# Performance work log

Measured on AMD Instinct MI355X. Metric: run time of the kernel, lower is better.

The kernel has to match this reference:

```python
import jax, jax.numpy as jnp
import numpy as np

N = 50000; E = 800000; B = 5000
ND = 32; ED = 16; HD = 64; H = 128; L = 3
IN_DIM = ND + 2 * H  # 288, GNN in_channels
NEG = 0.2  # GATv2 leaky_relu slope
EPS = 1e-5  # LayerNorm eps


def silu(x):
    return x * jax.nn.sigmoid(x)


def layer_norm(x, g, b):
    mu = jnp.mean(x, -1, keepdims=True)
    v = jnp.var(x, -1, keepdims=True)
    return (x - mu) * jax.lax.rsqrt(v + EPS) * g + b


def setup_inputs() -> dict:
    key = jax.random.key(0)
    ks = iter(jax.random.split(key, 48))

    def w(shape):
        return jax.random.normal(next(ks), shape, jnp.float32) * 0.02

    inp = {}
    inp['x_t'] = jax.random.normal(next(ks), (N, ND), jnp.float32)
    inp['t'] = jax.random.randint(next(ks), (N,), 0, 1000)
    inp['household_features'] = jax.random.normal(next(ks), (B, HD), jnp.float32)
    inp['edge_index'] = jax.random.randint(next(ks), (2, E), 0, N)
    inp['edge_attr'] = jax.random.normal(next(ks), (E, ED), jnp.float32)
    inp['batch'] = jnp.sort(jax.random.randint(next(ks), (N,), 0, B))
    z = jnp.zeros; o = jnp.ones
    inp.update(dict(
        tW1=w((1, H)), tb1=z(H), tW2=w((H, H)), tb2=z(H),
        hW1=w((HD, H)), hb1=z(H), hg1=o(H), hB1=z(H),
        hW2=w((H, H)), hb2=z(H), hg2=o(H), hB2=z(H),
        Wl=w((L, IN_DIM, H)), bl=z((L, H)), Wr=w((L, IN_DIM, H)), br=z((L, H)),
        We=w((L, ED, H)), att=w((L, H)), gb=z((L, H)),
        fcpW=w((H, IN_DIM)), fcpb=z(IN_DIM),
        npW1=w((H, H)), npb1=z(H), npg=o(H), npB=z(H),
        npW2=w((H, ND)), npb2=z(ND)))
    return inp


def reference(x_t, t, household_features, edge_index, edge_attr, batch,
              tW1, tb1, tW2, tb2,
              hW1, hb1, hg1, hB1, hW2, hb2, hg2, hB2,
              Wl, bl, Wr, br, We, att, gb,
              fcpW, fcpb, npW1, npb1, npg, npB, npW2, npb2):
    # time embedding: Linear(1,H) -> SiLU -> Linear(H,H)
    t_emb = silu(t[:, None].astype(jnp.float32) @ tW1 + tb1) @ tW2 + tb2
    # household encoder: (Linear, LN, SiLU) x2, then gather per node
    h = silu(layer_norm(household_features @ hW1 + hb1, hg1, hB1))
    h = silu(layer_norm(h @ hW2 + hb2, hg2, hB2))
    x = jnp.concatenate([x_t, t_emb, h[batch]], axis=1)  # [N, IN_DIM]

    # add self loops (PyG default), edge_attr filled with per-feature mean
    loop = jnp.arange(N)
    src = jnp.concatenate([edge_index[0], loop])
    dst = jnp.concatenate([edge_index[1], loop])
    ea = jnp.concatenate([edge_attr, jnp.broadcast_to(edge_attr.mean(0), (N, ED))], axis=0)

    for l in range(L):  # GATv2Conv layers (heads=1)
        xl = x @ Wl[l] + bl[l]  # [N, H] source transform
        xr = x @ Wr[l] + br[l]  # [N, H] target transform
        m = jax.nn.leaky_relu(xl[src] + xr[dst] + ea @ We[l], NEG)  # [Etot, H]
        score = m @ att[l]  # [Etot]
        smax = jax.ops.segment_max(score, dst, num_segments=N)
        ex = jnp.exp(score - smax[dst])
        denom = jax.ops.segment_sum(ex, dst, num_segments=N) + 1e-16
        alpha = ex / denom[dst]
        out = jax.ops.segment_sum(alpha[:, None] * xl[src], dst, num_segments=N) + gb[l]
        x = silu(out)
        if l < L - 1:
            x = x @ fcpW + fcpb  # fc_projection back to IN_DIM
    # node_projection: Linear, LN, SiLU, Linear
    return silu(layer_norm(x @ npW1 + npb1, npg, npB)) @ npW2 + npb2
```

## Files before the change

kernel.cpp:

```cpp
#include <hip/hip_runtime.h>
#include <hip/hip_bf16.h>

#define NN 50000
#define NE 800000
#define NB 5000
#define ND 32
#define EDD 16
#define HDD 64
#define H 128
#define ETOT (NE + NN)
#define NEG 0.2f
#define EPS_LN 1e-5f

__device__ __forceinline__ float siluf(float x){ return x / (1.f + __expf(-x)); }

__device__ __forceinline__ float wsum(float v){
  v += __shfl_xor(v, 32, 64);
  v += __shfl_xor(v, 16, 64);
  v += __shfl_xor(v, 8, 64);
  v += __shfl_xor(v, 4, 64);
  v += __shfl_xor(v, 2, 64);
  v += __shfl_xor(v, 1, 64);
  return v;
}

__device__ __forceinline__ float blockLN128(float x, const float* g, const float* b, int j, float* red){
  int lane = j & 63, wid = j >> 6;
  float s = wsum(x);
  if (lane == 0) red[wid] = s;
  __syncthreads();
  float mu = (red[0] + red[1]) * 0.0078125f;
  float d = x - mu;
  float s2 = wsum(d * d);
  if (lane == 0) red[2 + wid] = s2;
  __syncthreads();
  float var = (red[2] + red[3]) * 0.0078125f;
  return d * (1.f / sqrtf(var + EPS_LN)) * g[j] + b[j];
}

__global__ __launch_bounds__(128) void k_house(const float* __restrict__ hf,
    const float* __restrict__ hW1, const float* __restrict__ hb1,
    const float* __restrict__ hg1, const float* __restrict__ hB1,
    const float* __restrict__ hW2, const float* __restrict__ hb2,
    const float* __restrict__ hg2, const float* __restrict__ hB2,
    float* __restrict__ hout){
  __shared__ float sin_[HDD];
  __shared__ float smid[H];
  __shared__ float red[4];
  int bidx = blockIdx.x, j = threadIdx.x;
  if (j < HDD) sin_[j] = hf[bidx * HDD + j];
  __syncthreads();
  float acc = hb1[j];
  #pragma unroll
  for (int k = 0; k < HDD; k++) acc += sin_[k] * hW1[k * H + j];
  float v = siluf(blockLN128(acc, hg1, hB1, j, red));
  __syncthreads();
  smid[j] = v;
  __syncthreads();
  float acc2 = hb2[j];
  #pragma unroll
  for (int k = 0; k < H; k++) acc2 += smid[k] * hW2[k * H + j];
  float v2 = siluf(blockLN128(acc2, hg2, hB2, j, red));
  hout[bidx * H + j] = v2;
}

__global__ __launch_bounds__(128) void k_temb(const float* __restrict__ tW1, const float* __restrict__ tb1,
    const float* __restrict__ tW2, const float* __restrict__ tb2, float* __restrict__ table){
  __shared__ float smid[H];
  int bidx = blockIdx.x, j = threadIdx.x;
  float tv = (float)bidx;
  smid[j] = siluf(tv * tW1[j] + tb1[j]);
  __syncthreads();
  float acc = tb2[j];
  #pragma unroll
  for (int k = 0; k < H; k++) acc += smid[k] * tW2[k * H + j];
  table[bidx * H + j] = acc;
}

__global__ __launch_bounds__(256) void k_gemm(const float* __restrict__ A, const float* __restrict__ W,
    const float* __restrict__ bias, float* __restrict__ C, int M, int K, int Nc){
  __shared__ float As[16][68];
  __shared__ float Ws[16][64];
  int t = threadIdx.x;
  int m0 = blockIdx.x * 64, n0 = blockIdx.y * 64;
  int tx = t & 15, ty = t >> 4;
  int la_m = t >> 2, la_k = (t & 3) << 2;
  int lw_k = t >> 4, lw_j = (t & 15) << 2;
  float acc[4][4] = {{0.f}};
  int arow = m0 + la_m;
  for (int k0 = 0; k0 < K; k0 += 16){
    float4 a = make_float4(0.f, 0.f, 0.f, 0.f);
    if (arow < M) a = *(const float4*)(A + (size_t)arow * K + k0 + la_k);
    As[la_k + 0][la_m] = a.x; As[la_k + 1][la_m] = a.y;
    As[la_k + 2][la_m] = a.z; As[la_k + 3][la_m] = a.w;
    float4 wv = make_float4(0.f, 0.f, 0.f, 0.f);
    if (n0 + lw_j < Nc) wv = *(const float4*)(W + (size_t)(k0 + lw_k) * Nc + n0 + lw_j);
    *(float4*)&Ws[lw_k][lw_j] = wv;
    __syncthreads();
    #pragma unroll
    for (int k = 0; k < 16; k++){
      float4 a4 = *(const float4*)&As[k][ty << 2];
      float4 b4 = *(const float4*)&Ws[k][tx << 2];
      acc[0][0] += a4.x * b4.x; acc[0][1] += a4.x * b4.y; acc[0][2] += a4.x * b4.z; acc[0][3] += a4.x * b4.w;
      acc[1][0] += a4.y * b4.x; acc[1][1] += a4.y * b4.y; acc[1][2] += a4.y * b4.z; acc[1][3] += a4.y * b4.w;
      acc[2][0] += a4.z * b4.x; acc[2][1] += a4.z * b4.y; acc[2][2] += a4.z * b4.z; acc[2][3] += a4.z * b4.w;
      acc[3][0] += a4.w * b4.x; acc[3][1] += a4.w * b4.y; acc[3][2] += a4.w * b4.z; acc[3][3] += a4.w * b4.w;
    }
    __syncthreads();
  }
  int col = n0 + (tx << 2);
  if (col < Nc){
    float4 b4 = make_float4(0.f, 0.f, 0.f, 0.f);
    if (bias) b4 = *(const float4*)(bias + col);
    #pragma unroll
    for (int r = 0; r < 4; r++){
      int row = m0 + (ty << 2) + r;
      if (row < M){
        float4 o = make_float4(acc[r][0] + b4.x, acc[r][1] + b4.y, acc[r][2] + b4.z, acc[r][3] + b4.w);
        *(float4*)(C + (size_t)row * Nc + col) = o;
      }
    }
  }
}

__global__ void k_pack0(const float* __restrict__ Wl, const float* __restrict__ Wr,
    float* __restrict__ Whead, float* __restrict__ Wmid, float* __restrict__ Wtail){
  int r = blockIdx.x, c = threadIdx.x;
  float v = (c < H) ? Wl[r * H + c] : Wr[r * H + (c - H)];
  if (r < 32) Whead[r * 256 + c] = v;
  else if (r < 160) Wmid[(r - 32) * 256 + c] = v;
  else Wtail[(r - 160) * 256 + c] = v;
}
__global__ void k_packW(const float* __restrict__ Wl, const float* __restrict__ Wr, float* __restrict__ Wp){
  int r = blockIdx.x, c = threadIdx.x;
  Wp[r * 256 + c] = (c < H) ? Wl[r * H + c] : Wr[r * H + (c - H)];
}
__global__ void k_bias0(const float* __restrict__ bl, const float* __restrict__ br, float* __restrict__ b0){
  int c = threadIdx.x;
  b0[c] = (c < H) ? bl[c] : br[c - H];
}
__global__ void k_cvec(const float* __restrict__ fcpb, const float* __restrict__ Wp,
    const float* __restrict__ bl, const float* __restrict__ br, float* __restrict__ cc){
  int c = threadIdx.x;
  float acc = (c < H) ? bl[c] : br[c - H];
  for (int k = 0; k < 288; k++) acc += fcpb[k] * Wp[k * 256 + c];
  cc[c] = acc;
}

__global__ __launch_bounds__(256) void k_xlr0(const float* __restrict__ x_t, const int* __restrict__ t,
    const int* __restrict__ batch, const float* __restrict__ T0, const float* __restrict__ H0,
    const float* __restrict__ Whead, const float* __restrict__ b0, float* __restrict__ xlr){
  __shared__ float sx[ND];
  __shared__ int sti, sbi;
  int i = blockIdx.x, c = threadIdx.x;
  if (c < ND) sx[c] = x_t[i * ND + c];
  if (c == 0){ sti = t[i]; sbi = batch[i]; }
  __syncthreads();
  float acc = b0[c] + T0[(size_t)sti * 256 + c] + H0[(size_t)sbi * 256 + c];
  #pragma unroll
  for (int k = 0; k < ND; k++) acc += sx[k] * Whead[k * 256 + c];
  xlr[(size_t)i * 256 + c] = acc;
}

__global__ void k_edge_mean(const float* __restrict__ ea, float* __restrict__ sum16){
  __shared__ float ss[16];
  int t = threadIdx.x;
  if (t < 16) ss[t] = 0.f;
  __syncthreads();
  float p[16];
  #pragma unroll
  for (int k = 0; k < 16; k++) p[k] = 0.f;
  for (int r = blockIdx.x * blockDim.x + t; r < NE; r += gridDim.x * blockDim.x){
    const float4* rp = (const float4*)(ea + (size_t)r * 16);
    float4 q0 = rp[0], q1 = rp[1], q2 = rp[2], q3 = rp[3];
    p[0] += q0.x; p[1] += q0.y; p[2] += q0.z; p[3] += q0.w;
    p[4] += q1.x; p[5] += q1.y; p[6] += q1.z; p[7] += q1.w;
    p[8] += q2.x; p[9] += q2.y; p[10] += q2.z; p[11] += q2.w;
    p[12] += q3.x; p[13] += q3.y; p[14] += q3.z; p[15] += q3.w;
  }
  #pragma unroll
  for (int k = 0; k < 16; k++) atomicAdd(&ss[k], p[k]);
  __syncthreads();
  if (t < 16) atomicAdd(&sum16[t], ss[t]);
}
__global__ void k_mean_scale(float* sum16){
  sum16[threadIdx.x] *= (1.f / NE);
}

__global__ void k_deg_init(int* __restrict__ deg){
  int i = blockIdx.x * 256 + threadIdx.x;
  if (i < NN) deg[i] = 1;
}
__global__ void k_deg_count(const int* __restrict__ eidx, int* __restrict__ deg){
  int e = blockIdx.x * 256 + threadIdx.x;
  if (e < NE) atomicAdd(&deg[eidx[NE + e]], 1);
}
__global__ __launch_bounds__(256) void k_scan1(const int* __restrict__ deg, int* __restrict__ row_ptr, int* __restrict__ bs){
  __shared__ int sc[256];
  int t = threadIdx.x;
  int base = blockIdx.x * 1024 + t * 4;
  int v0 = (base + 0 < NN) ? deg[base + 0] : 0;
  int v1 = (base + 1 < NN) ? deg[base + 1] : 0;
  int v2 = (base + 2 < NN) ? deg[base + 2] : 0;
  int v3 = (base + 3 < NN) ? deg[base + 3] : 0;
  int s0 = v0, s1 = s0 + v1, s2 = s1 + v2, s3 = s2 + v3;
  sc[t] = s3;
  __syncthreads();
  for (int off = 1; off < 256; off <<= 1){
    int add = (t >= off) ? sc[t - off] : 0;
    __syncthreads();
    sc[t] += add;
    __syncthreads();
  }
  int excl = sc[t] - s3;
  if (base + 0 < NN) row_ptr[base + 1] = excl + s0;
  if (base + 1 < NN) row_ptr[base + 2] = excl + s1;
  if (base + 2 < NN) row_ptr[base + 3] = excl + s2;
  if (base + 3 < NN) row_ptr[base + 4] = excl + s3;
  if (t == 255) bs[blockIdx.x] = sc[255];
}
__global__ void k_scan2(int* __restrict__ bs, int nb){
  int lane = threadIdx.x;
  int v = (lane < nb) ? bs[lane] : 0;
  for (int off = 1; off < 64; off <<= 1){
    int n = __shfl_up(v, off, 64);
    if (lane >= off) v += n;
  }
  if (lane < nb) bs[lane] = v;
}
__global__ void k_scan3(int* __restrict__ row_ptr, const int* __restrict__ bs){
  int i = blockIdx.x * 256 + threadIdx.x;
  if (i == 0) row_ptr[0] = 0;
  if (i < NN){
    int chunk = i >> 10;
    if (chunk > 0) row_ptr[i + 1] += bs[chunk - 1];
  }
}
__global__ void k_fill_init(const int* __restrict__ row_ptr, int* __restrict__ fill){
  int i = blockIdx.x * 256 + threadIdx.x;
  if (i < NN) fill[i] = row_ptr[i];
}
__global__ void k_fill_edges(const int* __restrict__ eidx, int* __restrict__ fill,
    int* __restrict__ csrc, int* __restrict__ ceid){
  int e = blockIdx.x * 256 + threadIdx.x;
  if (e < NE){
    int d = eidx[NE + e];
    int pos = atomicAdd(&fill[d], 1);
    csrc[pos] = eidx[e];
    ceid[pos] = e;
  }
}
__global__ void k_fill_self(int* __restrict__ fill, int* __restrict__ csrc, int* __restrict__ ceid){
  int i = blockIdx.x * 256 + threadIdx.x;
  if (i < NN){
    int pos = atomicAdd(&fill[i], 1);
    csrc[pos] = i;
    ceid[pos] = NE;
  }
}

__global__ __launch_bounds__(256) void k_sagg(const float* __restrict__ xlr,
    const float* __restrict__ ea, const float* __restrict__ eamean,
    const float* __restrict__ Wel, const float* __restrict__ attl, const float* __restrict__ gbl,
    const int* __restrict__ row_ptr, const int* __restrict__ csrc, const int* __restrict__ ceid,
    float* __restrict__ y){
  int t = threadIdx.x;
  int wid = t >> 6, lane = t & 63;
  int i = blockIdx.x * 4 + wid;
  if (i >= NN) return;
  int dim = lane << 1;
  float2 rW[16];
  #pragma unroll
  for (int k = 0; k < 16; k++) rW[k] = *(const float2*)(Wel + k * H + dim);
  float ewm0 = 0.f, ewm1 = 0.f;
  #pragma unroll
  for (int k = 0; k < 16; k++){ float mk = eamean[k]; ewm0 += mk * rW[k].x; ewm1 += mk * rW[k].y; }
  float2 xr = *(const float2*)(xlr + (size_t)i * 256 + H + dim);
  float a0 = attl[dim], a1 = attl[dim + 1];
  int row = __builtin_amdgcn_readfirstlane(row_ptr[i]);
  int end = __builtin_amdgcn_readfirstlane(row_ptr[i + 1]);
  float m = -1e30f, den = 0.f, ax = 0.f, ay = 0.f;
  for (int p = row; p < end; ++p){
    int s   = __builtin_amdgcn_readfirstlane(csrc[p]);
    int eid = __builtin_amdgcn_readfirstlane(ceid[p]);
    float2 vl = *(const float2*)(xlr + (size_t)s * 256 + dim);
    float ew0, ew1;
    if (eid < NE){
      const float* ep = ea + (size_t)eid * 16;
      ew0 = 0.f; ew1 = 0.f;
      #pragma unroll
      for (int k = 0; k < 16; k++){ float evk = ep[k]; ew0 += evk * rW[k].x; ew1 += evk * rW[k].y; }
    } else { ew0 = ewm0; ew1 = ewm1; }
    float vx = vl.x + xr.x + ew0;
    float vy = vl.y + xr.y + ew1;
    vx = fmaxf(vx, NEG * vx);
    vy = fmaxf(vy, NEG * vy);
    float sc = wsum(a0 * vx + a1 * vy);
    float newm = fmaxf(m, sc);
    float scale = __expf(m - newm);
    float wv = __expf(sc - newm);
    den = den * scale + wv;
    ax = ax * scale + wv * vl.x;
    ay = ay * scale + wv * vl.y;
    m = newm;
  }
  float inv = 1.f / (den + 1e-16f);
  float ox = siluf(ax * inv + gbl[dim]);
  float oy = siluf(ay * inv + gbl[dim + 1]);
  *(float2*)(y + (size_t)i * H + dim) = make_float2(ox, oy);
}

__global__ __launch_bounds__(128) void k_ln_silu(const float* __restrict__ z, const float* __restrict__ g,
    const float* __restrict__ b, float* __restrict__ z2){
  __shared__ float red[4];
  int i = blockIdx.x, j = threadIdx.x;
  float x = z[(size_t)i * H + j];
  float v = blockLN128(x, g, b, j, red);
  z2[(size_t)i * H + j] = siluf(v);
}

extern "C" void kernel_launch(void* const* d_in, const int* in_sizes, int n_in,
                              void* d_out, int out_size, void* d_ws, size_t ws_size,
                              hipStream_t stream){
  (void)in_sizes; (void)n_in; (void)out_size; (void)ws_size;
  const float* x_t  = (const float*)d_in[0];
  const int*   t    = (const int*)d_in[1];
  const float* hf   = (const float*)d_in[2];
  const int*   eidx = (const int*)d_in[3];
  const float* ea   = (const float*)d_in[4];
  const int*   batch= (const int*)d_in[5];
  const float* tW1  = (const float*)d_in[6];
  const float* tb1  = (const float*)d_in[7];
  const float* tW2  = (const float*)d_in[8];
  const float* tb2  = (const float*)d_in[9];
  const float* hW1  = (const float*)d_in[10];
  const float* hb1  = (const float*)d_in[11];
  const float* hg1  = (const float*)d_in[12];
  const float* hB1  = (const float*)d_in[13];
  const float* hW2  = (const float*)d_in[14];
  const float* hb2  = (const float*)d_in[15];
  const float* hg2  = (const float*)d_in[16];
  const float* hB2  = (const float*)d_in[17];
  const float* Wl   = (const float*)d_in[18];
  const float* bl   = (const float*)d_in[19];
  const float* Wr   = (const float*)d_in[20];
  const float* br   = (const float*)d_in[21];
  const float* We   = (const float*)d_in[22];
  const float* att  = (const float*)d_in[23];
  const float* gb   = (const float*)d_in[24];
  const float* fcpW = (const float*)d_in[25];
  const float* fcpb = (const float*)d_in[26];
  const float* npW1 = (const float*)d_in[27];
  const float* npb1 = (const float*)d_in[28];
  const float* npg  = (const float*)d_in[29];
  const float* npB  = (const float*)d_in[30];
  const float* npW2 = (const float*)d_in[31];
  const float* npb2 = (const float*)d_in[32];

  char* w = (char*)d_ws;
  size_t off = 0;
  auto alloc = [&](size_t bytes) -> void* {
    void* p = w + off;
    off += (bytes + 255) & ~(size_t)255;
    return p;
  };
  float* table = (float*)alloc((size_t)1000 * H * 4);
  float* hbuf  = (float*)alloc((size_t)NB * H * 4);
  float* T0    = (float*)alloc((size_t)1000 * 256 * 4);
  float* H0b   = (float*)alloc((size_t)NB * 256 * 4);
  float* W0h   = (float*)alloc((size_t)32 * 256 * 4);
  float* W0m   = (float*)alloc((size_t)128 * 256 * 4);
  float* W0t   = (float*)alloc((size_t)128 * 256 * 4);
  float* b0    = (float*)alloc(256 * 4);
  float* Wp1   = (float*)alloc((size_t)288 * 256 * 4);
  float* Wp2   = (float*)alloc((size_t)288 * 256 * 4);
  float* Ac1   = (float*)alloc((size_t)128 * 256 * 4);
  float* Ac2   = (float*)alloc((size_t)128 * 256 * 4);
  float* cc1   = (float*)alloc(256 * 4);
  float* cc2   = (float*)alloc(256 * 4);
  float* eam   = (float*)alloc(16 * 4);
  int* deg     = (int*)alloc((size_t)NN * 4);
  int* row_ptr = (int*)alloc((size_t)(NN + 1) * 4);
  int* fill    = (int*)alloc((size_t)NN * 4);
  int* bs      = (int*)alloc(64 * 4);
  int* csrc    = (int*)alloc((size_t)ETOT * 4);
  int* ceid    = (int*)alloc((size_t)ETOT * 4);
  float* xlr   = (float*)alloc((size_t)NN * 256 * 4);
  float* y     = (float*)alloc((size_t)NN * H * 4);
  float* z  = xlr;
  float* z2 = xlr + (size_t)NN * H;

  hipMemsetAsync(eam, 0, 64, stream);
  k_edge_mean<<<512, 256, 0, stream>>>(ea, eam);
  k_mean_scale<<<1, 16, 0, stream>>>(eam);
  k_house<<<NB, 128, 0, stream>>>(hf, hW1, hb1, hg1, hB1, hW2, hb2, hg2, hB2, hbuf);
  k_temb<<<1000, 128, 0, stream>>>(tW1, tb1, tW2, tb2, table);
  k_deg_init<<<(NN + 255) / 256, 256, 0, stream>>>(deg);
  k_deg_count<<<(NE + 255) / 256, 256, 0, stream>>>(eidx, deg);
  k_scan1<<<49, 256, 0, stream>>>(deg, row_ptr, bs);
  k_scan2<<<1, 64, 0, stream>>>(bs, 49);
  k_scan3<<<(NN + 255) / 256, 256, 0, stream>>>(row_ptr, bs);
  k_fill_init<<<(NN + 255) / 256, 256, 0, stream>>>(row_ptr, fill);
  k_fill_edges<<<(NE + 255) / 256, 256, 0, stream>>>(eidx, fill, csrc, ceid);
  k_fill_self<<<(NN + 255) / 256, 256, 0, stream>>>(fill, csrc, ceid);
  k_pack0<<<288, 256, 0, stream>>>(Wl, Wr, W0h, W0m, W0t);
  k_bias0<<<1, 256, 0, stream>>>(bl, br, b0);
  k_packW<<<288, 256, 0, stream>>>(Wl + 1 * 288 * H, Wr + 1 * 288 * H, Wp1);
  k_packW<<<288, 256, 0, stream>>>(Wl + 2 * 288 * H, Wr + 2 * 288 * H, Wp2);
  k_cvec<<<1, 256, 0, stream>>>(fcpb, Wp1, bl + H, br + H, cc1);
  k_cvec<<<1, 256, 0, stream>>>(fcpb, Wp2, bl + 2 * H, br + 2 * H, cc2);
  auto gemm = [&](const float* A, const float* W_, const float* bias, float* C, int M, int K, int Nc){
    dim3 g((M + 63) / 64, (Nc + 63) / 64);
    k_gemm<<<g, 256, 0, stream>>>(A, W_, bias, C, M, K, Nc);
  };
  gemm(table, W0m, nullptr, T0, 1000, H, 256);
  gemm(hbuf, W0t, nullptr, H0b, NB, H, 256);
  gemm(fcpW, Wp1, nullptr, Ac1, H, 288, 256);
  gemm(fcpW, Wp2, nullptr, Ac2, H, 288, 256);
  k_xlr0<<<NN, 256, 0, stream>>>(x_t, t, batch, T0, H0b, W0h, b0, xlr);
  k_sagg<<<(NN + 3) / 4, 256, 0, stream>>>(xlr, ea, eam, We, att, gb, row_ptr, csrc, ceid, y);
  gemm(y, Ac1, cc1, xlr, NN, H, 256);
  k_sagg<<<(NN + 3) / 4, 256, 0, stream>>>(xlr, ea, eam, We + 16 * H, att + H, gb + H, row_ptr, csrc, ceid, y);
  gemm(y, Ac2, cc2, xlr, NN, H, 256);
  k_sagg<<<(NN + 3) / 4, 256, 0, stream>>>(xlr, ea, eam, We + 32 * H, att + 2 * H, gb + 2 * H, row_ptr, csrc, ceid, y);
  gemm(y, npW1, npb1, z, NN, H, H);
  k_ln_silu<<<NN, 128, 0, stream>>>(z, npg, npB, z2);
  gemm(z2, npW2, npb2, (float*)d_out, NN, H, ND);
}
```

Before: 1.025 ms.

## Prefetch next edge in GAT aggregation and add 128x128 GEMM tile kernel

The aggregation loop now software-pipelines the next edge's source row and edge-attribute vector loads, so they are in flight while the current edge is processed. It loads edge attributes as float4 vectors and reads the precomputed mean vector as if it were a regular edge. The online softmax update is split into two branches so each edge needs only one exp. A separate 128x128-tile, 8x8-per-thread GEMM kernel replaces the 64x64 GEMM for the large N-row projections, giving more reuse per thread at the cost of more registers and lower occupancy.

Result: slower. 1.059 ms (+3.4%).

```diff
diff --git a/kernel.cpp b/kernel.cpp
--- a/kernel.cpp
+++ b/kernel.cpp
@@ -123,6 +123,67 @@
   }
 }
 
+__global__ __launch_bounds__(256) void k_gemm128(const float* __restrict__ A, const float* __restrict__ W,
+    const float* __restrict__ bias, float* __restrict__ C, int M, int K, int Nc){
+  __shared__ float As[16][132];
+  __shared__ float Ws[16][128];
+  int t = threadIdx.x;
+  int m0 = blockIdx.x * 128, n0 = blockIdx.y * 128;
+  int tx = t & 15, ty = t >> 4;
+  float acc[8][8];
+  #pragma unroll
+  for (int r = 0; r < 8; r++)
+    #pragma unroll
+    for (int c = 0; c < 8; c++) acc[r][c] = 0.f;
+  for (int k0 = 0; k0 < K; k0 += 16){
+    #pragma unroll
+    for (int l = 0; l < 2; l++){
+      int idx = t + l * 256;
+      int ar = idx >> 2, ac = (idx & 3) << 2;
+      float4 a = make_float4(0.f, 0.f, 0.f, 0.f);
+      if (m0 + ar < M) a = *(const float4*)(A + (size_t)(m0 + ar) * K + k0 + ac);
+      As[ac + 0][ar] = a.x; As[ac + 1][ar] = a.y;
+      As[ac + 2][ar] = a.z; As[ac + 3][ar] = a.w;
+    }
+    #pragma unroll
+    for (int l = 0; l < 2; l++){
+      int idx = t + l * 256;
+      int wr = idx >> 5, wc = (idx & 31) << 2;
+      float4 wv = make_float4(0.f, 0.f, 0.f, 0.f);
+      if (n0 + wc < Nc) wv = *(const float4*)(W + (size_t)(k0 + wr) * Nc + n0 + wc);
+      *(float4*)&Ws[wr][wc] = wv;
+    }
+    __syncthreads();
+    #pragma unroll
+    for (int k = 0; k < 16; k++){
+      float4 a0 = *(const float4*)&As[k][ty * 8];
+      float4 a1 = *(const float4*)&As[k][ty * 8 + 4];
+      float4 b0 = *(const float4*)&Ws[k][tx * 8];
+      float4 b1 = *(const float4*)&Ws[k][tx * 8 + 4];
+      float ar_[8] = {a0.x, a0.y, a0.z, a0.w, a1.x, a1.y, a1.z, a1.w};
+      float bc_[8] = {b0.x, b0.y, b0.z, b0.w, b1.x, b1.y, b1.z, b1.w};
+      #pragma unroll
+      for (int r = 0; r < 8; r++)
+        #pragma unroll
+        for (int c = 0; c < 8; c++) acc[r][c] += ar_[r] * bc_[c];
+    }
+    __syncthreads();
+  }
+  int col = n0 + tx * 8;
+  float4 bb0 = make_float4(0.f, 0.f, 0.f, 0.f), bb1 = bb0;
+  if (bias && col < Nc){ bb0 = *(const float4*)(bias + col); bb1 = *(const float4*)(bias + col + 4); }
+  #pragma unroll
+  for (int r = 0; r < 8; r++){
+    int row = m0 + ty * 8 + r;
+    if (row < M && col < Nc){
+      float4 o0 = make_float4(acc[r][0] + bb0.x, acc[r][1] + bb0.y, acc[r][2] + bb0.z, acc[r][3] + bb0.w);
+      float4 o1 = make_float4(acc[r][4] + bb1.x, acc[r][5] + bb1.y, acc[r][6] + bb1.z, acc[r][7] + bb1.w);
+      *(float4*)(C + (size_t)row * Nc + col) = o0;
+      *(float4*)(C + (size_t)row * Nc + col + 4) = o1;
+    }
+  }
+}
+
 __global__ void k_pack0(const float* __restrict__ Wl, const float* __restrict__ Wr,
     float* __restrict__ Whead, float* __restrict__ Wmid, float* __restrict__ Wtail){
   int r = blockIdx.x, c = threadIdx.x;
@@ -272,37 +333,50 @@
   float2 rW[16];
   #pragma unroll
   for (int k = 0; k < 16; k++) rW[k] = *(const float2*)(Wel + k * H + dim);
-  float ewm0 = 0.f, ewm1 = 0.f;
-  #pragma unroll
-  for (int k = 0; k < 16; k++){ float mk = eamean[k]; ewm0 += mk * rW[k].x; ewm1 += mk * rW[k].y; }
   float2 xr = *(const float2*)(xlr + (size_t)i * 256 + H + dim);
   float a0 = attl[dim], a1 = attl[dim + 1];
   int row = __builtin_amdgcn_readfirstlane(row_ptr[i]);
   int end = __builtin_amdgcn_readfirstlane(row_ptr[i + 1]);
   float m = -1e30f, den = 0.f, ax = 0.f, ay = 0.f;
+  int s_c = __builtin_amdgcn_readfirstlane(csrc[row]);
+  int e_c = __builtin_amdgcn_readfirstlane(ceid[row]);
+  float2 vl_c = *(const float2*)(xlr + (size_t)s_c * 256 + dim);
+  const float* ep_c = (e_c < NE) ? (ea + (size_t)e_c * 16) : eamean;
+  float4 q0 = *(const float4*)(ep_c);
+  float4 q1 = *(const float4*)(ep_c + 4);
+  float4 q2 = *(const float4*)(ep_c + 8);
+  float4 q3 = *(const float4*)(ep_c + 12);
   for (int p = row; p < end; ++p){
-    int s   = __builtin_amdgcn_readfirstlane(csrc[p]);
-    int eid = __builtin_amdgcn_readfirstlane(ceid[p]);
-    float2 vl = *(const float2*)(xlr + (size_t)s * 256 + dim);
-    float ew0, ew1;
-    if (eid < NE){
-      const float* ep = ea + (size_t)eid * 16;
-      ew0 = 0.f; ew1 = 0.f;
-      #pragma unroll
-      for (int k = 0; k < 16; k++){ float evk = ep[k]; ew0 += evk * rW[k].x; ew1 += evk * rW[k].y; }
-    } else { ew0 = ewm0; ew1 = ewm1; }
-    float vx = vl.x + xr.x + ew0;
-    float vy = vl.y + xr.y + ew1;
+    int pn = (p + 1 < end) ? (p + 1) : p;
+    int s_n = __builtin_amdgcn_readfirstlane(csrc[pn]);
+    int e_n = __builtin_amdgcn_readfirstlane(ceid[pn]);
+    float2 vl_n = *(const float2*)(xlr + (size_t)s_n * 256 + dim);
+    const float* ep_n = (e_n < NE) ? (ea + (size_t)e_n * 16) : eamean;
+    float4 n0 = *(const float4*)(ep_n);
+    float4 n1 = *(const float4*)(ep_n + 4);
+    float4 n2 = *(const float4*)(ep_n + 8);
+    float4 n3 = *(const float4*)(ep_n + 12);
+    float eav[16] = {q0.x, q0.y, q0.z, q0.w, q1.x, q1.y, q1.z, q1.w,
+                     q2.x, q2.y, q2.z, q2.w, q3.x, q3.y, q3.z, q3.w};
+    float ew0 = 0.f, ew1 = 0.f;
+    #pragma unroll
+    for (int k = 0; k < 16; k++){ ew0 += eav[k] * rW[k].x; ew1 += eav[k] * rW[k].y; }
+    float vx = vl_c.x + xr.x + ew0;
+    float vy = vl_c.y + xr.y + ew1;
     vx = fmaxf(vx, NEG * vx);
     vy = fmaxf(vy, NEG * vy);
     float sc = wsum(a0 * vx + a1 * vy);
-    float newm = fmaxf(m, sc);
-    float scale = __expf(m - newm);
-    float wv = __expf(sc - newm);
-    den = den * scale + wv;
-    ax = ax * scale + wv * vl.x;
-    ay = ay * scale + wv * vl.y;
-    m = newm;
+    if (sc <= m){
+      float wv = __expf(sc - m);
+      den += wv; ax += wv * vl_c.x; ay += wv * vl_c.y;
+    } else {
+      float scale = __expf(m - sc);
+      den = den * scale + 1.f;
+      ax = ax * scale + vl_c.x;
+      ay = ay * scale + vl_c.y;
+      m = sc;
+    }
+    vl_c = vl_n; q0 = n0; q1 = n1; q2 = n2; q3 = n3;
   }
   float inv = 1.f / (den + 1e-16f);
   float ox = siluf(ax * inv + gbl[dim]);
@@ -413,17 +487,21 @@
     dim3 g((M + 63) / 64, (Nc + 63) / 64);
     k_gemm<<<g, 256, 0, stream>>>(A, W_, bias, C, M, K, Nc);
   };
-  gemm(table, W0m, nullptr, T0, 1000, H, 256);
-  gemm(hbuf, W0t, nullptr, H0b, NB, H, 256);
+  auto gemm128 = [&](const float* A, const float* W_, const float* bias, float* C, int M, int K, int Nc){
+    dim3 g((M + 127) / 128, (Nc + 127) / 128);
+    k_gemm128<<<g, 256, 0, stream>>>(A, W_, bias, C, M, K, Nc);
+  };
+  gemm128(table, W0m, nullptr, T0, 1000, H, 256);
+  gemm128(hbuf, W0t, nullptr, H0b, NB, H, 256);
   gemm(fcpW, Wp1, nullptr, Ac1, H, 288, 256);
   gemm(fcpW, Wp2, nullptr, Ac2, H, 288, 256);
   k_xlr0<<<NN, 256, 0, stream>>>(x_t, t, batch, T0, H0b, W0h, b0, xlr);
   k_sagg<<<(NN + 3) / 4, 256, 0, stream>>>(xlr, ea, eam, We, att, gb, row_ptr, csrc, ceid, y);
-  gemm(y, Ac1, cc1, xlr, NN, H, 256);
+  gemm128(y, Ac1, cc1, xlr, NN, H, 256);
   k_sagg<<<(NN + 3) / 4, 256, 0, stream>>>(xlr, ea, eam, We + 16 * H, att + H, gb + H, row_ptr, csrc, ceid, y);
-  gemm(y, Ac2, cc2, xlr, NN, H, 256);
+  gemm128(y, Ac2, cc2, xlr, NN, H, 256);
   k_sagg<<<(NN + 3) / 4, 256, 0, stream>>>(xlr, ea, eam, We + 32 * H, att + 2 * H, gb + 2 * H, row_ptr, csrc, ceid, y);
-  gemm(y, npW1, npb1, z, NN, H, H);
+  gemm128(y, npW1, npb1, z, NN, H, H);
   k_ln_silu<<<NN, 128, 0, stream>>>(z, npg, npB, z2);
   gemm(z2, npW2, npb2, (float*)d_out, NN, H, ND);
 }
```
